# Kernel optimization log

Measured on AMD Instinct MI355X. Metric: run time of the kernel, lower is better.

Reference implementation:

```python
import jax, jax.numpy as jnp
import numpy as np

ALPHA = 0.1

def setup_inputs() -> dict:
    key = jax.random.key(0)
    ks = jax.random.split(key, 7)
    T, N, H, Din, Dinit, Dout = 512, 256, 512, 2, 2, 2
    return {
        "initdir": jax.random.normal(ks[0], (1, N, Dinit), dtype=jnp.float32),
        "velocities": jax.random.normal(ks[1], (T, N, Din), dtype=jnp.float32),
        "fc_w": jax.random.normal(ks[2], (H, Dinit), dtype=jnp.float32) * (0.1 / np.sqrt(H)),
        "fc_b": jax.random.normal(ks[3], (H,), dtype=jnp.float32) * 0.01,
        "W_in": jax.random.normal(ks[4], (Din, H), dtype=jnp.float32) * (0.1 / np.sqrt(Din)),
        "W_rec": jax.random.normal(ks[5], (H, H), dtype=jnp.float32) * (0.1 / np.sqrt(H)),
        "W_out": jax.random.normal(ks[6], (H, Dout), dtype=jnp.float32) * (0.1 / np.sqrt(H)),
        "bias": jnp.zeros((H,), dtype=jnp.float32),
    }

def reference(initdir, velocities, fc_w, fc_b, W_in, W_rec, W_out, bias):
    # h0 = fc(initdir.squeeze(0))  -> (N, H)
    h0 = initdir[0] @ fc_w.T + fc_b

    def step(prevH, x_t):
        # leaky integration: h = (1-a)*prevH + a*(relu(tanh(prevH)) @ W_rec + x @ W_in + b)
        act = jax.nn.relu(jnp.tanh(prevH))
        h = (1.0 - ALPHA) * prevH + ALPHA * (act @ W_rec + x_t @ W_in + bias)
        return h, h

    _, hs = jax.lax.scan(step, h0, velocities)  # hs: (T, N, H)
    out = jax.nn.relu(jnp.tanh(hs)) @ W_out     # (T, N, Dout)
    return out
```

## Files before the change

kernel.cpp:

```cpp
#include <hip/hip_runtime.h>
#include <math.h>

#define TT 512
#define NN 256
#define HH 512
constexpr float AL = 0.1f;

typedef unsigned int uint;
typedef unsigned long long u64;
typedef unsigned short u16;
typedef _Float16 f16;
typedef f16 f16x8 __attribute__((ext_vector_type(8)));
typedef float f32x4 __attribute__((ext_vector_type(4)));
using half2v = decltype(__builtin_amdgcn_cvt_pkrtz(0.0f, 0.0f));

struct Args {
  const float* initdir; const float* vel; const float* fc_w; const float* fc_b;
  const float* W_in; const float* W_rec; const float* W_out; const float* bias;
  float* out; uint* pbuf;
};

__global__ void zero_pbuf(u64* p) { p[blockIdx.x * 512 + threadIdx.x] = 0ull; }
__global__ void zero_out(float4* p) { p[blockIdx.x * 512 + threadIdx.x] = float4{0,0,0,0}; }

__global__ __launch_bounds__(512, 1)
void rnn_kernel(Args a) {
  __shared__ alignas(16) u16 actw[2][HH];
  __shared__ float pred[2][256];

  const int tid = threadIdx.x;
  const int wav = tid >> 6, lan = tid & 63;
  const int bid = blockIdx.x;
  const int kk = bid >> 3;
  const int c = kk & 1;
  const int grp = (bid & 7) * 16 + (kk >> 1);
  const int own0 = c * 256, fo0 = (1 - c) * 256;

  const int g = tid >> 8, jj = tid & 255;
  const int ucol = own0 + jj, ugn = grp * 2 + g;

  const int l15 = lan & 15, gq = lan >> 4;
  const int ncol0 = own0 + wav * 32 + l15;

  f16x8 B0[16], B1[16];
#pragma unroll
  for (int kb = 0; kb < 16; ++kb) {
#pragma unroll
    for (int j = 0; j < 8; ++j) {
      const int k = kb * 32 + gq * 8 + j;
      B0[kb][j] = (f16)a.W_rec[(size_t)k * HH + ncol0];
      B1[kb][j] = (f16)a.W_rec[(size_t)k * HH + ncol0 + 16];
    }
  }

  const float fw0 = a.fc_w[ucol * 2], fw1 = a.fc_w[ucol * 2 + 1], fb = a.fc_b[ucol];
  const float wi0 = AL * a.W_in[ucol], wi1 = AL * a.W_in[HH + ucol];
  const float bj = AL * a.bias[ucol];
  const float wo0 = a.W_out[ucol * 2], wo1 = a.W_out[ucol * 2 + 1];
  const float id0 = a.initdir[ugn * 2], id1 = a.initdir[ugn * 2 + 1];

  uint* shipb = a.pbuf + (size_t)(bid ^ 8) * 1024;
  const uint* pollb = a.pbuf + (size_t)bid * 1024;
  const float2* velp = (const float2*)a.vel;
  float* outf = a.out;

  float h = fmaf(id0, fw0, fmaf(id1, fw1, fb));
  {
    const float act = fmaxf(tanhf(h), 0.0f);
    const uint pk = __builtin_bit_cast(uint, __builtin_amdgcn_cvt_pkrtz(act, 0.f)) & 0xffffu;
    actw[g][ucol] = (u16)pk;
    __hip_atomic_store(shipb + 0 * 512 + tid, (pk << 16) | 1u,
                       __ATOMIC_RELAXED, __HIP_MEMORY_SCOPE_AGENT);
  }

  const u16* arow = &actw[(l15 < 2) ? l15 : 0][0];

  for (int t = 0; t < TT; ++t) {
    const float2 xv = velp[t * NN + ugn];
    const int par = t & 1;

    {
      const uint want = (uint)(t + 1);
      const uint* slot = pollb + par * 512 + tid;
      uint v;
      do {
        v = __hip_atomic_load(slot, __ATOMIC_RELAXED, __HIP_MEMORY_SCOPE_AGENT);
      } while ((v & 0xffffu) != want);
      actw[g][fo0 + jj] = (u16)(v >> 16);
    }
    __syncthreads();

    f32x4 ac0 = {0.f, 0.f, 0.f, 0.f}, ac1 = {0.f, 0.f, 0.f, 0.f};
#pragma unroll
    for (int kb = 0; kb < 16; ++kb) {
      const f16x8 A = *(const f16x8*)(arow + kb * 32 + gq * 8);
      ac0 = __builtin_amdgcn_mfma_f32_16x16x32_f16(A, B0[kb], ac0, 0, 0, 0);
      ac1 = __builtin_amdgcn_mfma_f32_16x16x32_f16(A, B1[kb], ac1, 0, 0, 0);
    }
    if (lan < 16) {
      const int col = wav * 32 + l15;
      pred[0][col] = ac0[0];
      pred[1][col] = ac0[1];
      pred[0][col + 16] = ac1[0];
      pred[1][col + 16] = ac1[1];
    }
    __syncthreads();

    const float y = pred[g][jj];
    h = fmaf(0.9f, h, fmaf(AL, y, fmaf(xv.x, wi0, fmaf(xv.y, wi1, bj))));
    const float act = fmaxf(tanhf(h), 0.0f);
    const uint pk = __builtin_bit_cast(uint, __builtin_amdgcn_cvt_pkrtz(act, 0.f)) & 0xffffu;
    actw[g][ucol] = (u16)pk;
    __hip_atomic_store(shipb + ((t + 1) & 1) * 512 + tid, (pk << 16) | (uint)(t + 2),
                       __ATOMIC_RELAXED, __HIP_MEMORY_SCOPE_AGENT);

    float q0 = act * wo0, q1 = act * wo1;
#pragma unroll
    for (int off = 32; off; off >>= 1) {
      q0 += __shfl_down(q0, off);
      q1 += __shfl_down(q1, off);
    }
    if (lan == 0) {
      atomicAdd(&outf[(t * NN + ugn) * 2 + 0], q0);
      atomicAdd(&outf[(t * NN + ugn) * 2 + 1], q1);
    }
  }
}

extern "C" void kernel_launch(void* const* d_in, const int* in_sizes, int n_in,
                              void* d_out, int out_size, void* d_ws, size_t ws_size,
                              hipStream_t stream) {
  (void)in_sizes; (void)n_in; (void)out_size; (void)ws_size;
  Args a;
  a.initdir = (const float*)d_in[0];
  a.vel     = (const float*)d_in[1];
  a.fc_w    = (const float*)d_in[2];
  a.fc_b    = (const float*)d_in[3];
  a.W_in    = (const float*)d_in[4];
  a.W_rec   = (const float*)d_in[5];
  a.W_out   = (const float*)d_in[6];
  a.bias    = (const float*)d_in[7];
  a.out     = (float*)d_out;
  a.pbuf    = (uint*)d_ws;

  zero_pbuf<<<256, 512, 0, stream>>>((u64*)a.pbuf);
  zero_out<<<128, 512, 0, stream>>>((float4*)d_out);

  void* args[] = { &a };
  hipLaunchCooperativeKernel((const void*)rnn_kernel, dim3(256), dim3(512),
                             args, 0, stream);
}
```

Measured before the change: 864.1 us.

## Repartition RNN across 8-block clusters with 8 sequences per block and packed exchange

Changes the work split so that each cluster of 8 blocks shares 8 sequences, with each block owning 64 hidden columns instead of a pair of blocks sharing 2 sequences. Each wave computes a 16-column by 256-row K-half MFMA tile, and the two K-halves are summed through shared memory. Activations are exchanged as packed half2 plus a tag in 64-bit words, and each thread polls four slots. The aim is to use more MFMA rows and cut weight registers per thread, at the cost of all-to-all exchange among 8 blocks per step, which adds cross-block latency.

```diff
diff --git a/kernel.cpp b/kernel.cpp
--- a/kernel.cpp
+++ b/kernel.cpp
@@ -12,46 +12,44 @@
 typedef _Float16 f16;
 typedef f16 f16x8 __attribute__((ext_vector_type(8)));
 typedef float f32x4 __attribute__((ext_vector_type(4)));
-using half2v = decltype(__builtin_amdgcn_cvt_pkrtz(0.0f, 0.0f));
 
 struct Args {
   const float* initdir; const float* vel; const float* fc_w; const float* fc_b;
   const float* W_in; const float* W_rec; const float* W_out; const float* bias;
-  float* out; uint* pbuf;
+  float* out; u64* pbuf;
 };
 
 __global__ void zero_pbuf(u64* p) { p[blockIdx.x * 512 + threadIdx.x] = 0ull; }
-__global__ void zero_out(float4* p) { p[blockIdx.x * 512 + threadIdx.x] = float4{0,0,0,0}; }
+__global__ void zero_out(float4* p) { p[blockIdx.x * 512 + threadIdx.x] = float4{0.f, 0.f, 0.f, 0.f}; }
 
 __global__ __launch_bounds__(512, 1)
 void rnn_kernel(Args a) {
-  __shared__ alignas(16) u16 actw[2][HH];
-  __shared__ float pred[2][256];
+  __shared__ alignas(16) u16 actw[8][520];
+  __shared__ float pred[2][8][64];
 
   const int tid = threadIdx.x;
   const int wav = tid >> 6, lan = tid & 63;
   const int bid = blockIdx.x;
-  const int kk = bid >> 3;
-  const int c = kk & 1;
-  const int grp = (bid & 7) * 16 + (kk >> 1);
-  const int own0 = c * 256, fo0 = (1 - c) * 256;
+  const int c = bid & 7;
+  const int ci = bid >> 3;
 
-  const int g = tid >> 8, jj = tid & 255;
-  const int ucol = own0 + jj, ugn = grp * 2 + g;
+  const int g = wav, jj = lan;
+  const int ucol = c * 64 + jj;
+  const int ugn = ci * 8 + g;
 
+  const int nt = wav & 3, h0 = wav >> 2;
   const int l15 = lan & 15, gq = lan >> 4;
-  const int ncol0 = own0 + wav * 32 + l15;
+  const int ncol = c * 64 + nt * 16 + l15;
+  const int arow = l15 & 7;
 
-  f16x8 B0[16], B1[16];
+  f16x8 B[8];
 #pragma unroll
-  for (int kb = 0; kb < 16; ++kb) {
+  for (int kb = 0; kb < 8; ++kb)
 #pragma unroll
     for (int j = 0; j < 8; ++j) {
-      const int k = kb * 32 + gq * 8 + j;
-      B0[kb][j] = (f16)a.W_rec[(size_t)k * HH + ncol0];
-      B1[kb][j] = (f16)a.W_rec[(size_t)k * HH + ncol0 + 16];
+      const int k = h0 * 256 + kb * 32 + gq * 8 + j;
+      B[kb][j] = (f16)a.W_rec[(size_t)k * HH + ncol];
     }
-  }
 
   const float fw0 = a.fc_w[ucol * 2], fw1 = a.fc_w[ucol * 2 + 1], fb = a.fc_b[ucol];
   const float wi0 = AL * a.W_in[ucol], wi1 = AL * a.W_in[HH + ucol];
@@ -59,60 +57,68 @@
   const float wo0 = a.W_out[ucol * 2], wo1 = a.W_out[ucol * 2 + 1];
   const float id0 = a.initdir[ugn * 2], id1 = a.initdir[ugn * 2 + 1];
 
-  uint* shipb = a.pbuf + (size_t)(bid ^ 8) * 1024;
-  const uint* pollb = a.pbuf + (size_t)bid * 1024;
+  float h = fmaf(id0, fw0, fmaf(id1, fw1, fb));
+
+  u64* reg0 = a.pbuf + (size_t)ci * 2048;
+  u64* reg1 = a.pbuf + (size_t)(32 + ci) * 2048;
+  const int shipw = g * 256 + c * 32 + (jj >> 1);
   const float2* velp = (const float2*)a.vel;
   float* outf = a.out;
 
-  float h = fmaf(id0, fw0, fmaf(id1, fw1, fb));
-  {
-    const float act = fmaxf(tanhf(h), 0.0f);
-    const uint pk = __builtin_bit_cast(uint, __builtin_amdgcn_cvt_pkrtz(act, 0.f)) & 0xffffu;
-    actw[g][ucol] = (u16)pk;
-    __hip_atomic_store(shipb + 0 * 512 + tid, (pk << 16) | 1u,
-                       __ATOMIC_RELAXED, __HIP_MEMORY_SCOPE_AGENT);
-  }
+  auto ship = [&](u64* reg, float act, uint tag) {
+    const float aR = __shfl_xor(act, 1);
+    if (!(jj & 1)) {
+      const uint d = __builtin_bit_cast(uint, __builtin_amdgcn_cvt_pkrtz(act, aR));
+      __hip_atomic_store(reg + shipw, (u64)d | ((u64)tag << 32),
+                         __ATOMIC_RELAXED, __HIP_MEMORY_SCOPE_AGENT);
+    }
+  };
 
-  const u16* arow = &actw[(l15 < 2) ? l15 : 0][0];
+  ship(reg0, fmaxf(tanhf(h), 0.0f), 1u);
 
   for (int t = 0; t < TT; ++t) {
     const float2 xv = velp[t * NN + ugn];
-    const int par = t & 1;
 
     {
+      const u64* s = ((t & 1) ? reg1 : reg0) + 4 * tid;
       const uint want = (uint)(t + 1);
-      const uint* slot = pollb + par * 512 + tid;
-      uint v;
-      do {
-        v = __hip_atomic_load(slot, __ATOMIC_RELAXED, __HIP_MEMORY_SCOPE_AGENT);
-      } while ((v & 0xffffu) != want);
-      actw[g][fo0 + jj] = (u16)(v >> 16);
+      u64 v0 = __hip_atomic_load(s + 0, __ATOMIC_RELAXED, __HIP_MEMORY_SCOPE_AGENT);
+      u64 v1 = __hip_atomic_load(s + 1, __ATOMIC_RELAXED, __HIP_MEMORY_SCOPE_AGENT);
+      u64 v2 = __hip_atomic_load(s + 2, __ATOMIC_RELAXED, __HIP_MEMORY_SCOPE_AGENT);
+      u64 v3 = __hip_atomic_load(s + 3, __ATOMIC_RELAXED, __HIP_MEMORY_SCOPE_AGENT);
+      for (;;) {
+        const bool b0 = (uint)(v0 >> 32) != want, b1 = (uint)(v1 >> 32) != want;
+        const bool b2 = (uint)(v2 >> 32) != want, b3 = (uint)(v3 >> 32) != want;
+        if (!(b0 | b1 | b2 | b3)) break;
+        if (b0) v0 = __hip_atomic_load(s + 0, __ATOMIC_RELAXED, __HIP_MEMORY_SCOPE_AGENT);
+        if (b1) v1 = __hip_atomic_load(s + 1, __ATOMIC_RELAXED, __HIP_MEMORY_SCOPE_AGENT);
+        if (b2) v2 = __hip_atomic_load(s + 2, __ATOMIC_RELAXED, __HIP_MEMORY_SCOPE_AGENT);
+        if (b3) v3 = __hip_atomic_load(s + 3, __ATOMIC_RELAXED, __HIP_MEMORY_SCOPE_AGENT);
+      }
+      *(uint4*)&actw[wav][8 * lan] =
+          make_uint4((uint)v0, (uint)v1, (uint)v2, (uint)v3);
     }
     __syncthreads();
 
-    f32x4 ac0 = {0.f, 0.f, 0.f, 0.f}, ac1 = {0.f, 0.f, 0.f, 0.f};
+    {
+      f32x4 acc = {0.f, 0.f, 0.f, 0.f};
 #pragma unroll
-    for (int kb = 0; kb < 16; ++kb) {
-      const f16x8 A = *(const f16x8*)(arow + kb * 32 + gq * 8);
-      ac0 = __builtin_amdgcn_mfma_f32_16x16x32_f16(A, B0[kb], ac0, 0, 0, 0);
-      ac1 = __builtin_amdgcn_mfma_f32_16x16x32_f16(A, B1[kb], ac1, 0, 0, 0);
-    }
-    if (lan < 16) {
-      const int col = wav * 32 + l15;
-      pred[0][col] = ac0[0];
-      pred[1][col] = ac0[1];
-      pred[0][col + 16] = ac1[0];
-      pred[1][col + 16] = ac1[1];
+      for (int kb = 0; kb < 8; ++kb) {
+        const f16x8 A = *(const f16x8*)&actw[arow][h0 * 256 + kb * 32 + gq * 8];
+        acc = __builtin_amdgcn_mfma_f32_16x16x32_f16(A, B[kb], acc, 0, 0, 0);
+      }
+      if (lan < 32) {
+        const int r0 = (lan >> 4) * 4, col = nt * 16 + l15;
+#pragma unroll
+        for (int r = 0; r < 4; ++r) pred[h0][r0 + r][col] = acc[r];
+      }
     }
     __syncthreads();
 
-    const float y = pred[g][jj];
+    const float y = pred[0][g][jj] + pred[1][g][jj];
     h = fmaf(0.9f, h, fmaf(AL, y, fmaf(xv.x, wi0, fmaf(xv.y, wi1, bj))));
     const float act = fmaxf(tanhf(h), 0.0f);
-    const uint pk = __builtin_bit_cast(uint, __builtin_amdgcn_cvt_pkrtz(act, 0.f)) & 0xffffu;
-    actw[g][ucol] = (u16)pk;
-    __hip_atomic_store(shipb + ((t + 1) & 1) * 512 + tid, (pk << 16) | (uint)(t + 2),
-                       __ATOMIC_RELAXED, __HIP_MEMORY_SCOPE_AGENT);
+    ship((t & 1) ? reg0 : reg1, act, (uint)(t + 2));
 
     float q0 = act * wo0, q1 = act * wo1;
 #pragma unroll
@@ -141,9 +147,9 @@
   a.W_out   = (const float*)d_in[6];
   a.bias    = (const float*)d_in[7];
   a.out     = (float*)d_out;
-  a.pbuf    = (uint*)d_ws;
+  a.pbuf    = (u64*)d_ws;
 
-  zero_pbuf<<<256, 512, 0, stream>>>((u64*)a.pbuf);
+  zero_pbuf<<<256, 512, 0, stream>>>(a.pbuf);
   zero_out<<<128, 512, 0, stream>>>((float4*)d_out);
 
   void* args[] = { &a };
```

New measurement: 1.361 ms. 57.5% more time.

## Split recurrent matmul into own/foreign halves to overlap partner wait

Applied to the files above, without the earlier changes.

The K dimension of the recurrent MFMA is split into the locally owned half and the half received from the partner block. The owned half is computed before spinning on the partner's flags, and the previous step's output projection is deferred into that wait window. Local activations are written to LDS as packed f16 pairs through a lane shuffle, with an extra barrier per step. This hides cross-block communication latency behind compute, at the cost of one more __syncthreads per timestep.

```diff
diff --git a/kernel.cpp b/kernel.cpp
--- a/kernel.cpp
+++ b/kernel.cpp
@@ -7,12 +7,10 @@
 constexpr float AL = 0.1f;
 
 typedef unsigned int uint;
-typedef unsigned long long u64;
 typedef unsigned short u16;
 typedef _Float16 f16;
 typedef f16 f16x8 __attribute__((ext_vector_type(8)));
 typedef float f32x4 __attribute__((ext_vector_type(4)));
-using half2v = decltype(__builtin_amdgcn_cvt_pkrtz(0.0f, 0.0f));
 
 struct Args {
   const float* initdir; const float* vel; const float* fc_w; const float* fc_b;
@@ -20,12 +18,12 @@
   float* out; uint* pbuf;
 };
 
-__global__ void zero_pbuf(u64* p) { p[blockIdx.x * 512 + threadIdx.x] = 0ull; }
-__global__ void zero_out(float4* p) { p[blockIdx.x * 512 + threadIdx.x] = float4{0,0,0,0}; }
+__global__ void zero_pbuf(uint* p) { p[blockIdx.x * 512 + threadIdx.x] = 0u; }
+__global__ void zero_out(float4* p) { p[blockIdx.x * 512 + threadIdx.x] = float4{0.f, 0.f, 0.f, 0.f}; }
 
 __global__ __launch_bounds__(512, 1)
 void rnn_kernel(Args a) {
-  __shared__ alignas(16) u16 actw[2][HH];
+  __shared__ uint actw32[2][256];
   __shared__ float pred[2][256];
 
   const int tid = threadIdx.x;
@@ -41,16 +39,20 @@
 
   const int l15 = lan & 15, gq = lan >> 4;
   const int ncol0 = own0 + wav * 32 + l15;
+  const int arow = (l15 < 2) ? l15 : 0;
 
-  f16x8 B0[16], B1[16];
+  f16x8 B0[2][8], B1[2][8];
 #pragma unroll
-  for (int kb = 0; kb < 16; ++kb) {
+  for (int hf = 0; hf < 2; ++hf) {
+    const int kb0 = (hf == 0) ? own0 : fo0;
 #pragma unroll
-    for (int j = 0; j < 8; ++j) {
-      const int k = kb * 32 + gq * 8 + j;
-      B0[kb][j] = (f16)a.W_rec[(size_t)k * HH + ncol0];
-      B1[kb][j] = (f16)a.W_rec[(size_t)k * HH + ncol0 + 16];
-    }
+    for (int kb = 0; kb < 8; ++kb)
+#pragma unroll
+      for (int j = 0; j < 8; ++j) {
+        const int k = kb0 + kb * 32 + gq * 8 + j;
+        B0[hf][kb][j] = (f16)a.W_rec[(size_t)k * HH + ncol0];
+        B1[hf][kb][j] = (f16)a.W_rec[(size_t)k * HH + ncol0 + 16];
+      }
   }
 
   const float fw0 = a.fc_w[ucol * 2], fw1 = a.fc_w[ucol * 2 + 1], fb = a.fc_b[ucol];
@@ -63,39 +65,70 @@
   const uint* pollb = a.pbuf + (size_t)bid * 1024;
   const float2* velp = (const float2*)a.vel;
   float* outf = a.out;
+  const u16* aw16 = (const u16*)actw32;
+
+  auto ship = [&](int par, float act, uint tag) {
+    const uint pk =
+        __builtin_bit_cast(uint, __builtin_amdgcn_cvt_pkrtz(act, 0.f)) & 0xffffu;
+    __hip_atomic_store(shipb + par * 512 + tid, (pk << 16) | tag,
+                       __ATOMIC_RELAXED, __HIP_MEMORY_SCOPE_AGENT);
+  };
+  auto own_lds = [&](float act) {
+    const float aR = __shfl_xor(act, 1);
+    if (!(jj & 1))
+      actw32[g][(own0 + jj) >> 1] =
+          __builtin_bit_cast(uint, __builtin_amdgcn_cvt_pkrtz(act, aR));
+  };
+  auto outproj = [&](int tt, float act) {
+    float q0 = act * wo0, q1 = act * wo1;
+#pragma unroll
+    for (int off = 32; off; off >>= 1) {
+      q0 += __shfl_down(q0, off);
+      q1 += __shfl_down(q1, off);
+    }
+    if (lan == 0) {
+      atomicAdd(&outf[(tt * NN + ugn) * 2 + 0], q0);
+      atomicAdd(&outf[(tt * NN + ugn) * 2 + 1], q1);
+    }
+  };
 
   float h = fmaf(id0, fw0, fmaf(id1, fw1, fb));
-  {
-    const float act = fmaxf(tanhf(h), 0.0f);
-    const uint pk = __builtin_bit_cast(uint, __builtin_amdgcn_cvt_pkrtz(act, 0.f)) & 0xffffu;
-    actw[g][ucol] = (u16)pk;
-    __hip_atomic_store(shipb + 0 * 512 + tid, (pk << 16) | 1u,
-                       __ATOMIC_RELAXED, __HIP_MEMORY_SCOPE_AGENT);
-  }
-
-  const u16* arow = &actw[(l15 < 2) ? l15 : 0][0];
+  float actv = fmaxf(tanhf(h), 0.0f);
+  ship(0, actv, 1u);
+  own_lds(actv);
+  __syncthreads();
 
   for (int t = 0; t < TT; ++t) {
     const float2 xv = velp[t * NN + ugn];
-    const int par = t & 1;
+    const uint want = (uint)(t + 1);
+    const uint* slot = pollb + (t & 1) * 512 + tid;
 
+    uint v = __hip_atomic_load(slot, __ATOMIC_RELAXED, __HIP_MEMORY_SCOPE_AGENT);
+
+    f32x4 ac0 = {0.f, 0.f, 0.f, 0.f}, ac1 = {0.f, 0.f, 0.f, 0.f};
+#pragma unroll
+    for (int kb = 0; kb < 8; ++kb) {
+      const f16x8 A = *(const f16x8*)(aw16 + arow * 512 + own0 + kb * 32 + gq * 8);
+      ac0 = __builtin_amdgcn_mfma_f32_16x16x32_f16(A, B0[0][kb], ac0, 0, 0, 0);
+      ac1 = __builtin_amdgcn_mfma_f32_16x16x32_f16(A, B1[0][kb], ac1, 0, 0, 0);
+    }
+
+    if (t > 0) outproj(t - 1, actv);
+
+    while ((v & 0xffffu) != want)
+      v = __hip_atomic_load(slot, __ATOMIC_RELAXED, __HIP_MEMORY_SCOPE_AGENT);
     {
-      const uint want = (uint)(t + 1);
-      const uint* slot = pollb + par * 512 + tid;
-      uint v;
-      do {
-        v = __hip_atomic_load(slot, __ATOMIC_RELAXED, __HIP_MEMORY_SCOPE_AGENT);
-      } while ((v & 0xffffu) != want);
-      actw[g][fo0 + jj] = (u16)(v >> 16);
+      const uint vO = __shfl_xor(v, 1);
+      if (!(jj & 1))
+        actw32[g][(fo0 + jj) >> 1] = (v >> 16) | (vO & 0xffff0000u);
     }
     __syncthreads();
 
-    f32x4 ac0 = {0.f, 0.f, 0.f, 0.f}, ac1 = {0.f, 0.f, 0.f, 0.f};
 #pragma unroll
-    for (int kb = 0; kb < 16; ++kb) {
-      const f16x8 A = *(const f16x8*)(arow + kb * 32 + gq * 8);
-      ac0 = __builtin_amdgcn_mfma_f32_16x16x32_f16(A, B0[kb], ac0, 0, 0, 0);
-      ac1 = __builtin_amdgcn_mfma_f32_16x16x32_f16(A, B1[kb], ac1, 0, 0, 0);
+    for (int kb = 0; kb < 8; ++kb) {
+      const f16x8 A = *(const f16x8*)(aw16 + arow * 512 + fo0 + kb * 32 + gq * 8);
+      ac0 = __builtin_amdgcn_mfma_f32_16x16x32_f16(A, B0[1][kb], ac0, 0, 0, 0);
+      ac1 = __builtin_amdgcn_mfma_f32_16x16x32_f16(A, B1[1][kb], ac1, 0, 0, 0);
     }
     if (lan < 16) {
       const int col = wav * 32 + l15;
@@ -108,23 +141,13 @@
 
     const float y = pred[g][jj];
     h = fmaf(0.9f, h, fmaf(AL, y, fmaf(xv.x, wi0, fmaf(xv.y, wi1, bj))));
-    const float act = fmaxf(tanhf(h), 0.0f);
-    const uint pk = __builtin_bit_cast(uint, __builtin_amdgcn_cvt_pkrtz(act, 0.f)) & 0xffffu;
-    actw[g][ucol] = (u16)pk;
-    __hip_atomic_store(shipb + ((t + 1) & 1) * 512 + tid, (pk << 16) | (uint)(t + 2),
-                       __ATOMIC_RELAXED, __HIP_MEMORY_SCOPE_AGENT);
+    actv = fmaxf(tanhf(h), 0.0f);
+    ship((t + 1) & 1, actv, (uint)(t + 2));
+    own_lds(actv);
+    __syncthreads();
+  }
 
-    float q0 = act * wo0, q1 = act * wo1;
-#pragma unroll
-    for (int off = 32; off; off >>= 1) {
-      q0 += __shfl_down(q0, off);
-      q1 += __shfl_down(q1, off);
-    }
-    if (lan == 0) {
-      atomicAdd(&outf[(t * NN + ugn) * 2 + 0], q0);
-      atomicAdd(&outf[(t * NN + ugn) * 2 + 1], q1);
-    }
-  }
+  outproj(TT - 1, actv);
 }
 
 extern "C" void kernel_launch(void* const* d_in, const int* in_sizes, int n_in,
@@ -143,7 +166,7 @@
   a.out     = (float*)d_out;
   a.pbuf    = (uint*)d_ws;
 
-  zero_pbuf<<<256, 512, 0, stream>>>((u64*)a.pbuf);
+  zero_pbuf<<<512, 512, 0, stream>>>(a.pbuf);
   zero_out<<<128, 512, 0, stream>>>((float4*)d_out);
 
   void* args[] = { &a };
```

Result: slower. 905.5 us (+4.8%).
